# Kernel optimization log

Hardware: AMD Instinct MI355X
Metric: run time of the kernel (lower is better)

## Reference

```python
import jax, jax.numpy as jnp
import numpy as np
import math

E = 64    # d_model = 2*feats
FF = 16   # dim_feedforward
F = 32    # feats
W = 100   # window_size
B = 128   # batch
NH = 32   # nhead = feats


def _mha(q_in, kv_in, w_qkv, b_qkv, w_o, b_o):
    # PyTorch nn.MultiheadAttention, seq-first layout [L, B, E]
    wq, wk, wv = jnp.split(w_qkv, 3, axis=0)
    bq, bk, bv = jnp.split(b_qkv, 3)
    q = q_in @ wq.T + bq
    k = kv_in @ wk.T + bk
    v = kv_in @ wv.T + bv
    L, Bb, _ = q.shape
    S = k.shape[0]
    hd = E // NH  # head_dim = 2
    qh = q.reshape(L, Bb, NH, hd)
    kh = k.reshape(S, Bb, NH, hd)
    vh = v.reshape(S, Bb, NH, hd)
    scores = jnp.einsum('lbhd,sbhd->bhls', qh, kh) / math.sqrt(hd)
    attn = jax.nn.softmax(scores, axis=-1)
    out = jnp.einsum('bhls,sbhd->lbhd', attn, vh).reshape(L, Bb, E)
    return out @ w_o.T + b_o


def _ffn(x, w1, b1, w2, b2):
    h = x @ w1.T + b1
    # nn.LeakyReLU(True) => negative_slope=True==1.0 => identity activation
    return h @ w2.T + b2


def _pos_encode(x):
    # pe[t,d] = sin(t*div[d]) + cos(t*div[d])  (both added, as in source)
    div = jnp.exp(jnp.arange(E, dtype=x.dtype) * (-math.log(10000.0) / E))
    pos = jnp.arange(x.shape[0], dtype=x.dtype)[:, None]
    pe = jnp.sin(pos * div) + jnp.cos(pos * div)  # [W, E]
    return x + pe[:, None, :]


def _encode(src, c, tgt, enc_p):
    (qkv_w, qkv_b, out_w, out_b, l1_w, l1_b, l2_w, l2_b) = enc_p
    s = jnp.concatenate([src, c], axis=2) * math.sqrt(F)
    s = _pos_encode(s)
    s = s + _mha(s, s, qkv_w, qkv_b, out_w, out_b)
    s = s + _ffn(s, l1_w, l1_b, l2_w, l2_b)
    t = jnp.tile(tgt, (1, 1, 2))
    return t, s


def _decode(t, mem, dec_p):
    (sa_qkv_w, sa_qkv_b, sa_out_w, sa_out_b,
     ca_qkv_w, ca_qkv_b, ca_out_w, ca_out_b,
     l1_w, l1_b, l2_w, l2_b) = dec_p
    t = t + _mha(t, t, sa_qkv_w, sa_qkv_b, sa_out_w, sa_out_b)
    t = t + _mha(t, mem, ca_qkv_w, ca_qkv_b, ca_out_w, ca_out_b)
    t = t + _ffn(t, l1_w, l1_b, l2_w, l2_b)
    return t


def _forward(src, tgt,
             enc_qkv_w, enc_qkv_b, enc_out_w, enc_out_b, enc_l1_w, enc_l1_b, enc_l2_w, enc_l2_b,
             d1_sa_qkv_w, d1_sa_qkv_b, d1_sa_out_w, d1_sa_out_b,
             d1_ca_qkv_w, d1_ca_qkv_b, d1_ca_out_w, d1_ca_out_b,
             d1_l1_w, d1_l1_b, d1_l2_w, d1_l2_b,
             d2_sa_qkv_w, d2_sa_qkv_b, d2_sa_out_w, d2_sa_out_b,
             d2_ca_qkv_w, d2_ca_qkv_b, d2_ca_out_w, d2_ca_out_b,
             d2_l1_w, d2_l1_b, d2_l2_w, d2_l2_b,
             fcn_w, fcn_b):
    enc_p = (enc_qkv_w, enc_qkv_b, enc_out_w, enc_out_b, enc_l1_w, enc_l1_b, enc_l2_w, enc_l2_b)
    d1_p = (d1_sa_qkv_w, d1_sa_qkv_b, d1_sa_out_w, d1_sa_out_b,
            d1_ca_qkv_w, d1_ca_qkv_b, d1_ca_out_w, d1_ca_out_b,
            d1_l1_w, d1_l1_b, d1_l2_w, d1_l2_b)
    d2_p = (d2_sa_qkv_w, d2_sa_qkv_b, d2_sa_out_w, d2_sa_out_b,
            d2_ca_qkv_w, d2_ca_qkv_b, d2_ca_out_w, d2_ca_out_b,
            d2_l1_w, d2_l1_b, d2_l2_w, d2_l2_b)
    fcn = lambda x: jax.nn.sigmoid(x @ fcn_w.T + fcn_b)

    c = jnp.zeros_like(src)
    t, mem = _encode(src, c, tgt, enc_p)
    x1 = fcn(_decode(t, mem, d1_p))
    c = (x1 - src) ** 2
    t, mem = _encode(src, c, tgt, enc_p)
    x2 = fcn(_decode(t, mem, d2_p))
    return x1, x2


def setup_inputs() -> dict:
    keys = jax.random.split(jax.random.key(0), 40)
    ki = iter(keys)

    def rn(shape, s=0.05):
        return jax.random.normal(next(ki), shape, dtype=jnp.float32) * s

    inp = {}
    inp['src'] = jax.random.normal(next(ki), (W, B, F), dtype=jnp.float32)
    inp['tgt'] = jax.random.normal(next(ki), (W, B, F), dtype=jnp.float32)
    for pfx in ['enc_', 'd1_sa_', 'd1_ca_', 'd2_sa_', 'd2_ca_']:
        inp[pfx + 'qkv_w'] = rn((3 * E, E))
        inp[pfx + 'qkv_b'] = rn((3 * E,))
        inp[pfx + 'out_w'] = rn((E, E))
        inp[pfx + 'out_b'] = rn((E,))
    for pfx in ['enc_', 'd1_', 'd2_']:
        inp[pfx + 'l1_w'] = rn((FF, E))
        inp[pfx + 'l1_b'] = rn((FF,))
        inp[pfx + 'l2_w'] = rn((E, FF))
        inp[pfx + 'l2_b'] = rn((E,))
    inp['fcn_w'] = rn((F, E))
    inp['fcn_b'] = rn((F,))
    return inp


def reference(src, tgt,
              enc_qkv_w, enc_qkv_b, enc_out_w, enc_out_b, enc_l1_w, enc_l1_b, enc_l2_w, enc_l2_b,
              d1_sa_qkv_w, d1_sa_qkv_b, d1_sa_out_w, d1_sa_out_b,
              d1_ca_qkv_w, d1_ca_qkv_b, d1_ca_out_w, d1_ca_out_b,
              d1_l1_w, d1_l1_b, d1_l2_w, d1_l2_b,
              d2_sa_qkv_w, d2_sa_qkv_b, d2_sa_out_w, d2_sa_out_b,
              d2_ca_qkv_w, d2_ca_qkv_b, d2_ca_out_w, d2_ca_out_b,
              d2_l1_w, d2_l1_b, d2_l2_w, d2_l2_b,
              fcn_w, fcn_b):
    return _forward(src, tgt,
                    enc_qkv_w, enc_qkv_b, enc_out_w, enc_out_b, enc_l1_w, enc_l1_b, enc_l2_w, enc_l2_b,
                    d1_sa_qkv_w, d1_sa_qkv_b, d1_sa_out_w, d1_sa_out_b,
                    d1_ca_qkv_w, d1_ca_qkv_b, d1_ca_out_w, d1_ca_out_b,
                    d1_l1_w, d1_l1_b, d1_l2_w, d1_l2_b,
                    d2_sa_qkv_w, d2_sa_qkv_b, d2_sa_out_w, d2_sa_out_b,
                    d2_ca_qkv_w, d2_ca_qkv_b, d2_ca_out_w, d2_ca_out_b,
                    d2_l1_w, d2_l1_b, d2_l2_w, d2_l2_b,
                    fcn_w, fcn_b)
```

## Files before the change

### kernel.cpp

```cpp
#include <hip/hip_runtime.h>
#include <math.h>


#define TPB 1024
#define RH 50
#define SQ32 5.656854249492381f

#ifndef __has_builtin
#define __has_builtin(x) 0
#endif
#if __has_builtin(__builtin_amdgcn_exp2f)
#define EXP2(x) __builtin_amdgcn_exp2f(x)
#else
#define EXP2(x) exp2f(x)
#endif

typedef float v4f __attribute__((ext_vector_type(4)));

struct KParams { const void* p[36]; };

template<int K, int MC>
__device__ __forceinline__ void ldw(const float* __restrict__ Wt, float* __restrict__ Ws, int tid)
{
    constexpr int WP = MC + 4;
    for (int i = tid; i < MC * K; i += TPB) {
        int m = i / K, k = i - m * K;
        Ws[k * WP + m] = Wt[i];
    }
}

template<int K, int WP>
__device__ __forceinline__ void gemm_row(const float* __restrict__ xrow,
                                         const float* __restrict__ wcol, float acc[4])
{
#pragma unroll 4
    for (int k = 0; k < K; ++k) {
        float xv = xrow[k];
        float4 w = *reinterpret_cast<const float4*>(wcol + k * WP);
        acc[0] = fmaf(xv, w.x, acc[0]);
        acc[1] = fmaf(xv, w.y, acc[1]);
        acc[2] = fmaf(xv, w.z, acc[2]);
        acc[3] = fmaf(xv, w.w, acc[3]);
    }
}

__device__ __forceinline__ void proj_q(const float* __restrict__ Xs, const float* __restrict__ W,
                                       const float* __restrict__ Bi, float* __restrict__ Q,
                                       float* __restrict__ RW, int tid)
{
    __syncthreads();
    ldw<64, 64>(W, RW, tid);
    __syncthreads();
    const int r0 = tid >> 4, cg = tid & 15;
    if (r0 < RH) {
        float a[4] = {0, 0, 0, 0};
        gemm_row<64, 68>(Xs + r0 * 68, RW + 4 * cg, a);
        float4 bb = *reinterpret_cast<const float4*>(Bi + 4 * cg);
        *reinterpret_cast<float4*>(Q + r0 * 68 + 4 * cg) =
            make_float4(a[0] + bb.x, a[1] + bb.y, a[2] + bb.z, a[3] + bb.w);
    }
}

__device__ __forceinline__ void proj_kv(const float* __restrict__ Xs, const float* __restrict__ W,
                                        const float* __restrict__ Bi, int off, int base,
                                        float4* __restrict__ KVs, float* __restrict__ RW, int tid)
{
    __syncthreads();
    ldw<64, 64>(W, RW, tid);
    __syncthreads();
    const int r0 = tid >> 4, cg = tid & 15;
    if (r0 < RH) {
        float a[4] = {0, 0, 0, 0};
        gemm_row<64, 68>(Xs + r0 * 68, RW + 4 * cg, a);
        float4 bb = *reinterpret_cast<const float4*>(Bi + 4 * cg);
        int sg = base + r0, h = 2 * cg;
        float* p0 = reinterpret_cast<float*>(KVs + h * 101 + sg);
        float* p1 = reinterpret_cast<float*>(KVs + (h + 1) * 101 + sg);
        *reinterpret_cast<float2*>(p0 + off) = make_float2(a[0] + bb.x, a[1] + bb.y);
        *reinterpret_cast<float2*>(p1 + off) = make_float2(a[2] + bb.z, a[3] + bb.w);
    }
}

__device__ __forceinline__ void kv_publish(float4* __restrict__ g, int* flagme, int stage,
                                           int base, int b, const float4* __restrict__ KVs, int tid)
{
    __syncthreads();
    for (int i = tid; i < 32 * RH; i += TPB) {
        int sl = i >> 5, h = i & 31, sg = base + sl;
        v4f v = *reinterpret_cast<const v4f*>(KVs + h * 101 + sg);
        float4* p = g + ((size_t)b * 100 + sg) * 32 + h;
        asm volatile("global_store_dwordx4 %0, %1, off sc0 sc1" :: "v"(p), "v"(v) : "memory");
    }
    asm volatile("s_waitcnt vmcnt(0)" ::: "memory");
    __syncthreads();
    if (tid == 0)
        asm volatile("global_store_dword %0, %1, off sc0 sc1" :: "v"(flagme), "v"(stage) : "memory");
}

__device__ __forceinline__ void kv_waitread(const float4* __restrict__ g, const int* flagpt,
                                            int stage, int pbase, int b,
                                            float4* __restrict__ KVs, int tid)
{
    if (tid == 0) {
        int f;
        for (;;) {
            asm volatile("global_load_dword %0, %1, off sc0 sc1\n\ts_waitcnt vmcnt(0)"
                         : "=v"(f) : "v"(flagpt) : "memory");
            if (f >= stage) break;
            __builtin_amdgcn_s_sleep(8);
        }
    }
    __syncthreads();
    for (int i = tid; i < 32 * RH; i += TPB) {
        int sl = i >> 5, h = i & 31, sg = pbase + sl;
        const float4* p = g + ((size_t)b * 100 + sg) * 32 + h;
        v4f v;
        asm volatile("global_load_dwordx4 %0, %1, off sc0 sc1\n\ts_waitcnt vmcnt(0)"
                     : "=v"(v) : "v"(p) : "memory");
        *reinterpret_cast<v4f*>(KVs + h * 101 + sg) = v;
    }
    __syncthreads();
}

__device__ __forceinline__ void attn_block(float* __restrict__ Q,
                                           const float4* __restrict__ KVs, int tid)
{
    __syncthreads();
    if (tid < 416) {
        const int h = tid / 13;
        const int g = tid - 13 * h;
        const int lq0 = 4 * g;
        const float4* kv = KVs + h * 101;
        const float SCALE = 0.7071067811865476f * 1.4426950408889634f;
        float q0[4], q1[4];
#pragma unroll
        for (int j = 0; j < 4; ++j) {
            if (lq0 + j < RH) {
                float2 qv = *reinterpret_cast<const float2*>(Q + (lq0 + j) * 68 + 2 * h);
                q0[j] = qv.x * SCALE; q1[j] = qv.y * SCALE;
            } else { q0[j] = 0.f; q1[j] = 0.f; }
        }
        float mx[4] = {-1e30f, -1e30f, -1e30f, -1e30f};
#pragma unroll 4
        for (int s = 0; s < 100; ++s) {
            float4 k = kv[s];
#pragma unroll
            for (int j = 0; j < 4; ++j)
                mx[j] = fmaxf(mx[j], fmaf(q0[j], k.x, q1[j] * k.y));
        }
        float sum[4] = {0, 0, 0, 0}, a0[4] = {0, 0, 0, 0}, a1[4] = {0, 0, 0, 0};
#pragma unroll 4
        for (int s = 0; s < 100; ++s) {
            float4 k = kv[s];
#pragma unroll
            for (int j = 0; j < 4; ++j) {
                float e = EXP2(fmaf(q0[j], k.x, fmaf(q1[j], k.y, -mx[j])));
                sum[j] += e;
                a0[j] = fmaf(e, k.z, a0[j]);
                a1[j] = fmaf(e, k.w, a1[j]);
            }
        }
#pragma unroll
        for (int j = 0; j < 4; ++j) {
            if (lq0 + j < RH) {
                float inv = 1.f / sum[j];
                *reinterpret_cast<float2*>(Q + (lq0 + j) * 68 + 2 * h) =
                    make_float2(a0[j] * inv, a1[j] * inv);
            }
        }
    }
    __syncthreads();
}

__device__ __forceinline__ void proj_out_res(const float* __restrict__ Ain, const float* __restrict__ W,
                                             const float* __restrict__ Bi, float* __restrict__ Sres,
                                             float* __restrict__ RW, int tid)
{
    __syncthreads();
    ldw<64, 64>(W, RW, tid);
    __syncthreads();
    const int r0 = tid >> 4, cg = tid & 15;
    if (r0 < RH) {
        float a[4] = {0, 0, 0, 0};
        gemm_row<64, 68>(Ain + r0 * 68, RW + 4 * cg, a);
        float4 bb = *reinterpret_cast<const float4*>(Bi + 4 * cg);
        float* sp = Sres + r0 * 68 + 4 * cg;
        float4 s0 = *reinterpret_cast<float4*>(sp);
        *reinterpret_cast<float4*>(sp) =
            make_float4(a[0] + bb.x + s0.x, a[1] + bb.y + s0.y,
                        a[2] + bb.z + s0.z, a[3] + bb.w + s0.w);
    }
    __syncthreads();
}

__device__ __forceinline__ void ffn_block(float* __restrict__ X,
                                          const float* __restrict__ W1, const float* __restrict__ B1,
                                          const float* __restrict__ W2, const float* __restrict__ B2,
                                          float* __restrict__ RW, float* __restrict__ H, int tid)
{
    __syncthreads();
    ldw<64, 16>(W1, RW, tid);
    __syncthreads();
    {
        const int r = tid >> 3, lp = tid & 7;
        if (r < RH) {
            float h0 = B1[2 * lp], h1 = B1[2 * lp + 1];
            const float* xrow = X + r * 68;
#pragma unroll 4
            for (int k = 0; k < 64; ++k) {
                float xv = xrow[k];
                h0 = fmaf(xv, RW[k * 20 + 2 * lp], h0);
                h1 = fmaf(xv, RW[k * 20 + 2 * lp + 1], h1);
            }
            H[r * 20 + 2 * lp] = h0;
            H[r * 20 + 2 * lp + 1] = h1;
        }
    }
    __syncthreads();
    ldw<16, 64>(W2, RW, tid);
    __syncthreads();
    const int r0 = tid >> 4, cg = tid & 15;
    if (r0 < RH) {
        float a[4] = {0, 0, 0, 0};
        gemm_row<16, 68>(H + r0 * 20, RW + 4 * cg, a);
        float4 bb = *reinterpret_cast<const float4*>(B2 + 4 * cg);
        float* xp = X + r0 * 68 + 4 * cg;
        float4 u = *reinterpret_cast<float4*>(xp);
        *reinterpret_cast<float4*>(xp) =
            make_float4(a[0] + bb.x + u.x, a[1] + bb.y + u.y,
                        a[2] + bb.z + u.z, a[3] + bb.w + u.w);
    }
    __syncthreads();
}

__global__ __launch_bounds__(TPB) void k_fused(KParams prm, float* __restrict__ outp,
                                               float4* __restrict__ kvx0,
                                               float4* __restrict__ kvx1,
                                               int* __restrict__ flags)
{
    __shared__ float R0[RH * 68];
    __shared__ float R1[RH * 68];
    __shared__ float R3[RH * 68];
    __shared__ float4 KV[32 * 101];
    __shared__ float RW[64 * 68];
    __shared__ float Hs[RH * 20];
    __shared__ float X1s[RH * 36];

    const int tid = threadIdx.x;
    const int b = blockIdx.x & 127;
    const int half = blockIdx.x >> 7;
    const int base = half * RH;
    const int pbase = RH - base;
    int* flagme = flags + (b * 2 + half) * 32;
    int* flagpt = flags + (b * 2 + (1 - half)) * 32;

    const float* src = (const float*)prm.p[0];
    const float* tgt = (const float*)prm.p[1];

    for (int pass = 0; pass < 2; ++pass) {
        const float* Weq  = (const float*)prm.p[2];
        const float* Beq  = (const float*)prm.p[3];
        const float* Weo  = (const float*)prm.p[4];
        const float* Beo  = (const float*)prm.p[5];
        const float* Wel1 = (const float*)prm.p[22];
        const float* Bel1 = (const float*)prm.p[23];
        const float* Wel2 = (const float*)prm.p[24];
        const float* Bel2 = (const float*)prm.p[25];
        const float* Wsa  = (const float*)prm.p[pass ? 14 : 6];
        const float* Bsa  = (const float*)prm.p[pass ? 15 : 7];
        const float* Wsao = (const float*)prm.p[pass ? 16 : 8];
        const float* Bsao = (const float*)prm.p[pass ? 17 : 9];
        const float* Wca  = (const float*)prm.p[pass ? 18 : 10];
        const float* Bca  = (const float*)prm.p[pass ? 19 : 11];
        const float* Wcao = (const float*)prm.p[pass ? 20 : 12];
        const float* Bcao = (const float*)prm.p[pass ? 21 : 13];
        const float* Wdl1 = (const float*)prm.p[pass ? 30 : 26];
        const float* Bdl1 = (const float*)prm.p[pass ? 31 : 27];
        const float* Wdl2 = (const float*)prm.p[pass ? 32 : 28];
        const float* Bdl2 = (const float*)prm.p[pass ? 33 : 29];
        const float* Wf   = (const float*)prm.p[34];
        const float* Bf   = (const float*)prm.p[35];
        float* outx = outp + (pass ? 409600 : 0);

        __syncthreads();
        for (int i = tid; i < RH * 64; i += TPB) {
            int l = i >> 6, d = i & 63;
            int lg = base + l;
            float sv = src[((size_t)lg * 128 + b) * 32 + (d & 31)];
            float v;
            if (d < 32) v = sv;
            else if (pass == 0) v = 0.f;
            else { float df = X1s[l * 36 + (d - 32)] - sv; v = df * df; }
            float div = __expf((float)d * -0.14391156831212787f);
            float pe = 1.4142135623730951f * __sinf((float)lg * div + 0.7853981633974483f);
            R0[l * 68 + d] = v * SQ32 + pe;
        }

        int st = pass * 3 + 1;
        float4* g = (st & 1) ? kvx1 : kvx0;
        proj_kv(R0, Weq + 4096, Beq + 64, 0, base, KV, RW, tid);
        proj_kv(R0, Weq + 8192, Beq + 128, 2, base, KV, RW, tid);
        kv_publish(g, flagme, st, base, b, KV, tid);
        proj_q(R0, Weq, Beq, R1, RW, tid);
        kv_waitread(g, flagpt, st, pbase, b, KV, tid);
        attn_block(R1, KV, tid);
        proj_out_res(R1, Weo, Beo, R0, RW, tid);
        ffn_block(R0, Wel1, Bel1, Wel2, Bel2, RW, Hs, tid);

        for (int i = tid; i < RH * 8; i += TPB) {
            int l = i >> 3, q4 = i & 7;
            int lg = base + l;
            float4 tv = *reinterpret_cast<const float4*>(tgt + ((size_t)lg * 128 + b) * 32 + 4 * q4);
            *reinterpret_cast<float4*>(R3 + l * 68 + 4 * q4) = tv;
            *reinterpret_cast<float4*>(R3 + l * 68 + 32 + 4 * q4) = tv;
        }

        st = pass * 3 + 2;
        g = (st & 1) ? kvx1 : kvx0;
        proj_kv(R3, Wsa + 4096, Bsa + 64, 0, base, KV, RW, tid);
        proj_kv(R3, Wsa + 8192, Bsa + 128, 2, base, KV, RW, tid);
        kv_publish(g, flagme, st, base, b, KV, tid);
        proj_q(R3, Wsa, Bsa, R1, RW, tid);
        kv_waitread(g, flagpt, st, pbase, b, KV, tid);
        attn_block(R1, KV, tid);
        proj_out_res(R1, Wsao, Bsao, R3, RW, tid);

        st = pass * 3 + 3;
        g = (st & 1) ? kvx1 : kvx0;
        proj_kv(R0, Wca + 4096, Bca + 64, 0, base, KV, RW, tid);
        proj_kv(R0, Wca + 8192, Bca + 128, 2, base, KV, RW, tid);
        kv_publish(g, flagme, st, base, b, KV, tid);
        proj_q(R3, Wca, Bca, R1, RW, tid);
        kv_waitread(g, flagpt, st, pbase, b, KV, tid);
        attn_block(R1, KV, tid);
        proj_out_res(R1, Wcao, Bcao, R3, RW, tid);
        ffn_block(R3, Wdl1, Bdl1, Wdl2, Bdl2, RW, Hs, tid);

        ldw<64, 32>(Wf, RW, tid);
        __syncthreads();
        {
            const int r = tid >> 3, lp = tid & 7;
            if (r < RH) {
                float a[4] = {0, 0, 0, 0};
                gemm_row<64, 36>(R3 + r * 68, RW + 4 * lp, a);
                float4 bb = *reinterpret_cast<const float4*>(Bf + 4 * lp);
                float o0 = 1.f / (1.f + __expf(-(a[0] + bb.x)));
                float o1 = 1.f / (1.f + __expf(-(a[1] + bb.y)));
                float o2 = 1.f / (1.f + __expf(-(a[2] + bb.z)));
                float o3 = 1.f / (1.f + __expf(-(a[3] + bb.w)));
                int rg = base + r;
                *reinterpret_cast<float4*>(outx + ((size_t)rg * 128 + b) * 32 + 4 * lp) =
                    make_float4(o0, o1, o2, o3);
                if (pass == 0)
                    *reinterpret_cast<float4*>(X1s + r * 36 + 4 * lp) =
                        make_float4(o0, o1, o2, o3);
            }
        }
    }
}

extern "C" void kernel_launch(void* const* d_in, const int* in_sizes, int n_in,
                              void* d_out, int out_size, void* d_ws, size_t ws_size,
                              hipStream_t stream)
{
    KParams prm;
    for (int i = 0; i < 36; ++i) prm.p[i] = d_in[i];
    float4* kvx0 = (float4*)d_ws;
    float4* kvx1 = kvx0 + 409600;
    int* flags = (int*)(kvx1 + 409600);
    k_fused<<<dim3(256), dim3(TPB), 0, stream>>>(prm, (float*)d_out, kvx0, kvx1, flags);
}
```

Measured before the change: 184.2 us.

## Pre-transpose weights in a prep kernel and read them from global memory in the fused kernel

A new prep kernel transposes all weight matrices once into workspace, so the fused kernel no longer copies each weight into shared memory behind barriers. The GEMMs now give each thread two rows with packed FMA and read weights straight from global memory (cache). K and V are published in separate buffers directly from the projection, which removes the separate publish pass. The attention tiling also changes to 7 queries per thread across 256 threads. The cost is an extra kernel launch and global or cache-latency-bound weight reads in place of shared-memory reads.

```diff
diff --git a/kernel.cpp b/kernel.cpp
--- a/kernel.cpp
+++ b/kernel.cpp
@@ -15,234 +15,270 @@
 #define EXP2(x) exp2f(x)
 #endif
 
+typedef float v2f __attribute__((ext_vector_type(2)));
 typedef float v4f __attribute__((ext_vector_type(4)));
 
 struct KParams { const void* p[36]; };
 
-template<int K, int MC>
-__device__ __forceinline__ void ldw(const float* __restrict__ Wt, float* __restrict__ Ws, int tid)
-{
-    constexpr int WP = MC + 4;
-    for (int i = tid; i < MC * K; i += TPB) {
-        int m = i / K, k = i - m * K;
-        Ws[k * WP + m] = Wt[i];
+#define WT_QKV(i) (12288 * (i))
+#define WT_OUT(i) (61440 + 4096 * (i))
+#define WT_L1(i)  (81920 + 1024 * (i))
+#define WT_L2(i)  (84992 + 1024 * (i))
+#define WT_FCN    88064
+
+static __device__ const int g_tbl[17][4] = {
+    {2, 192, 6, 0},     {6, 192, 6, 12288}, {10, 192, 6, 24576},
+    {14, 192, 6, 36864},{18, 192, 6, 49152},
+    {4, 64, 6, 61440},  {8, 64, 6, 65536},  {12, 64, 6, 69632},
+    {16, 64, 6, 73728}, {20, 64, 6, 77824},
+    {22, 16, 6, 81920}, {26, 16, 6, 82944}, {30, 16, 6, 83968},
+    {24, 64, 4, 84992}, {28, 64, 4, 86016}, {32, 64, 4, 87040},
+    {34, 32, 6, 88064}};
+
+__global__ __launch_bounds__(256) void k_prep(KParams prm, float* __restrict__ wt)
+{
+    const int e = blockIdx.x;
+    const float* src = (const float*)prm.p[g_tbl[e][0]];
+    const int M = g_tbl[e][1], ks = g_tbl[e][2], dst = g_tbl[e][3];
+    const int N = M << ks, km = (1 << ks) - 1;
+    for (int i = threadIdx.x; i < N; i += 256) {
+        int m = i >> ks, k = i & km;
+        wt[dst + k * M + m] = src[i];
     }
 }
 
 template<int K, int WP>
-__device__ __forceinline__ void gemm_row(const float* __restrict__ xrow,
-                                         const float* __restrict__ wcol, float acc[4])
+__device__ __forceinline__ void gemm24(const float* __restrict__ x0,
+                                       const float* __restrict__ x1,
+                                       const float* __restrict__ gw, v2f acc[4])
 {
 #pragma unroll 4
-    for (int k = 0; k < K; ++k) {
-        float xv = xrow[k];
-        float4 w = *reinterpret_cast<const float4*>(wcol + k * WP);
-        acc[0] = fmaf(xv, w.x, acc[0]);
-        acc[1] = fmaf(xv, w.y, acc[1]);
-        acc[2] = fmaf(xv, w.z, acc[2]);
-        acc[3] = fmaf(xv, w.w, acc[3]);
-    }
-}
-
-__device__ __forceinline__ void proj_q(const float* __restrict__ Xs, const float* __restrict__ W,
-                                       const float* __restrict__ Bi, float* __restrict__ Q,
-                                       float* __restrict__ RW, int tid)
-{
-    __syncthreads();
-    ldw<64, 64>(W, RW, tid);
-    __syncthreads();
+    for (int kk = 0; kk < K / 4; ++kk) {
+        v4f xa = *reinterpret_cast<const v4f*>(x0 + 4 * kk);
+        v4f xb = *reinterpret_cast<const v4f*>(x1 + 4 * kk);
+#pragma unroll
+        for (int j = 0; j < 4; ++j) {
+            v4f w = *reinterpret_cast<const v4f*>(gw + (size_t)(4 * kk + j) * WP);
+            v2f xj = {xa[j], xb[j]};
+#pragma unroll
+            for (int c = 0; c < 4; ++c) {
+                v2f wc = {w[c], w[c]};
+                acc[c] = __builtin_elementwise_fma(xj, wc, acc[c]);
+            }
+        }
+    }
+}
+
+template<int K, int WP>
+__device__ __forceinline__ void gemm14(const float* __restrict__ x,
+                                       const float* __restrict__ gw, float acc[4])
+{
+#pragma unroll 4
+    for (int kk = 0; kk < K / 4; ++kk) {
+        v4f xv = *reinterpret_cast<const v4f*>(x + 4 * kk);
+#pragma unroll
+        for (int j = 0; j < 4; ++j) {
+            v4f w = *reinterpret_cast<const v4f*>(gw + (size_t)(4 * kk + j) * WP);
+#pragma unroll
+            for (int c = 0; c < 4; ++c) acc[c] = fmaf(xv[j], w[c], acc[c]);
+        }
+    }
+}
+
+__device__ __forceinline__ void kv_stage(const float* __restrict__ Xkv,
+    const float* __restrict__ gw ,
+    const float* __restrict__ Bi, int b, int base,
+    float2* __restrict__ Ks, float2* __restrict__ Vs,
+    float2* __restrict__ Kg, float2* __restrict__ Vg, int tid)
+{
+    if (tid >= 800) return;
+    const int c = (tid >= 400) ? 2 : 1;
+    const int u = tid - ((c == 2) ? 400 : 0);
+    const int r0 = u >> 4, cg = u & 15;
+    v2f acc[4] = {};
+    gemm24<64, 192>(Xkv + r0 * 68, Xkv + (r0 + 25) * 68, gw + c * 64 + 4 * cg, acc);
+    v4f bb = *reinterpret_cast<const v4f*>(Bi + c * 64 + 4 * cg);
+    float2* Ls = (c == 1) ? Ks : Vs;
+    float2* Lg = (c == 1) ? Kg : Vg;
+    const int h0 = 2 * cg;
+#pragma unroll
+    for (int rr = 0; rr < 2; ++rr) {
+        int sg = base + r0 + 25 * rr;
+        float2 p0 = make_float2(acc[0][rr] + bb[0], acc[1][rr] + bb[1]);
+        float2 p1 = make_float2(acc[2][rr] + bb[2], acc[3][rr] + bb[3]);
+        Ls[h0 * 102 + sg] = p0;
+        Ls[(h0 + 1) * 102 + sg] = p1;
+        v4f gv = {p0.x, p0.y, p1.x, p1.y};
+        float2* gp = Lg + ((size_t)b * 100 + sg) * 32 + h0;
+        asm volatile("global_store_dwordx4 %0, %1, off sc0 sc1" :: "v"(gp), "v"(gv) : "memory");
+    }
+}
+
+__device__ __forceinline__ void flag_pub(int* flagme, int st, int tid)
+{
+    asm volatile("s_waitcnt vmcnt(0)" ::: "memory");
+    __syncthreads();
+    if (tid == 0)
+        asm volatile("global_store_dword %0, %1, off sc0 sc1" :: "v"(flagme), "v"(st) : "memory");
+}
+
+__device__ __forceinline__ void q_stage(const float* __restrict__ Xq,
+    const float* __restrict__ gw, const float* __restrict__ Bi,
+    float* __restrict__ Q, int tid)
+{
+    if (tid >= 400) return;
     const int r0 = tid >> 4, cg = tid & 15;
-    if (r0 < RH) {
-        float a[4] = {0, 0, 0, 0};
-        gemm_row<64, 68>(Xs + r0 * 68, RW + 4 * cg, a);
-        float4 bb = *reinterpret_cast<const float4*>(Bi + 4 * cg);
-        *reinterpret_cast<float4*>(Q + r0 * 68 + 4 * cg) =
-            make_float4(a[0] + bb.x, a[1] + bb.y, a[2] + bb.z, a[3] + bb.w);
-    }
-}
-
-__device__ __forceinline__ void proj_kv(const float* __restrict__ Xs, const float* __restrict__ W,
-                                        const float* __restrict__ Bi, int off, int base,
-                                        float4* __restrict__ KVs, float* __restrict__ RW, int tid)
-{
-    __syncthreads();
-    ldw<64, 64>(W, RW, tid);
-    __syncthreads();
-    const int r0 = tid >> 4, cg = tid & 15;
-    if (r0 < RH) {
-        float a[4] = {0, 0, 0, 0};
-        gemm_row<64, 68>(Xs + r0 * 68, RW + 4 * cg, a);
-        float4 bb = *reinterpret_cast<const float4*>(Bi + 4 * cg);
-        int sg = base + r0, h = 2 * cg;
-        float* p0 = reinterpret_cast<float*>(KVs + h * 101 + sg);
-        float* p1 = reinterpret_cast<float*>(KVs + (h + 1) * 101 + sg);
-        *reinterpret_cast<float2*>(p0 + off) = make_float2(a[0] + bb.x, a[1] + bb.y);
-        *reinterpret_cast<float2*>(p1 + off) = make_float2(a[2] + bb.z, a[3] + bb.w);
-    }
-}
-
-__device__ __forceinline__ void kv_publish(float4* __restrict__ g, int* flagme, int stage,
-                                           int base, int b, const float4* __restrict__ KVs, int tid)
-{
-    __syncthreads();
-    for (int i = tid; i < 32 * RH; i += TPB) {
-        int sl = i >> 5, h = i & 31, sg = base + sl;
-        v4f v = *reinterpret_cast<const v4f*>(KVs + h * 101 + sg);
-        float4* p = g + ((size_t)b * 100 + sg) * 32 + h;
-        asm volatile("global_store_dwordx4 %0, %1, off sc0 sc1" :: "v"(p), "v"(v) : "memory");
-    }
-    asm volatile("s_waitcnt vmcnt(0)" ::: "memory");
-    __syncthreads();
-    if (tid == 0)
-        asm volatile("global_store_dword %0, %1, off sc0 sc1" :: "v"(flagme), "v"(stage) : "memory");
-}
-
-__device__ __forceinline__ void kv_waitread(const float4* __restrict__ g, const int* flagpt,
-                                            int stage, int pbase, int b,
-                                            float4* __restrict__ KVs, int tid)
+    v2f acc[4] = {};
+    gemm24<64, 192>(Xq + r0 * 68, Xq + (r0 + 25) * 68, gw + 4 * cg, acc);
+    v4f bb = *reinterpret_cast<const v4f*>(Bi + 4 * cg);
+#pragma unroll
+    for (int rr = 0; rr < 2; ++rr) {
+        v4f o = {acc[0][rr] + bb[0], acc[1][rr] + bb[1],
+                 acc[2][rr] + bb[2], acc[3][rr] + bb[3]};
+        *reinterpret_cast<v4f*>(Q + (r0 + 25 * rr) * 68 + 4 * cg) = o;
+    }
+}
+
+__device__ __forceinline__ void kv_wait(const int* flagpt, int st,
+    const float2* __restrict__ Kg, const float2* __restrict__ Vg,
+    int b, int pbase, float2* __restrict__ Ks, float2* __restrict__ Vs, int tid)
 {
     if (tid == 0) {
         int f;
         for (;;) {
             asm volatile("global_load_dword %0, %1, off sc0 sc1\n\ts_waitcnt vmcnt(0)"
                          : "=v"(f) : "v"(flagpt) : "memory");
-            if (f >= stage) break;
+            if (f >= st) break;
             __builtin_amdgcn_s_sleep(8);
         }
     }
     __syncthreads();
-    for (int i = tid; i < 32 * RH; i += TPB) {
-        int sl = i >> 5, h = i & 31, sg = pbase + sl;
-        const float4* p = g + ((size_t)b * 100 + sg) * 32 + h;
+    for (int i = tid; i < 1600; i += TPB) {
+        const int isV = i >= 800;
+        const int j = i - (isV ? 800 : 0);
+        const int sl = j >> 4, hp = j & 15;
+        const int sg = pbase + sl;
+        const float2* gp = (isV ? Vg : Kg) + ((size_t)b * 100 + sg) * 32 + 2 * hp;
         v4f v;
         asm volatile("global_load_dwordx4 %0, %1, off sc0 sc1\n\ts_waitcnt vmcnt(0)"
-                     : "=v"(v) : "v"(p) : "memory");
-        *reinterpret_cast<v4f*>(KVs + h * 101 + sg) = v;
+                     : "=v"(v) : "v"(gp) : "memory");
+        float2* Ls = isV ? Vs : Ks;
+        Ls[(2 * hp) * 102 + sg] = make_float2(v[0], v[1]);
+        Ls[(2 * hp + 1) * 102 + sg] = make_float2(v[2], v[3]);
     }
     __syncthreads();
 }
 
 __device__ __forceinline__ void attn_block(float* __restrict__ Q,
-                                           const float4* __restrict__ KVs, int tid)
-{
-    __syncthreads();
-    if (tid < 416) {
-        const int h = tid / 13;
-        const int g = tid - 13 * h;
-        const int lq0 = 4 * g;
-        const float4* kv = KVs + h * 101;
+    const float2* __restrict__ Ks, const float2* __restrict__ Vs, int tid)
+{
+    if (tid < 256) {
+        const int h = tid >> 3, g = tid & 7;
+        const int lq0 = 7 * g;
+        const int nq = (lq0 + 7 <= RH) ? 7 : (RH - lq0);
+        const v4f* K4 = reinterpret_cast<const v4f*>(Ks + h * 102);
+        const v4f* V4 = reinterpret_cast<const v4f*>(Vs + h * 102);
         const float SCALE = 0.7071067811865476f * 1.4426950408889634f;
-        float q0[4], q1[4];
-#pragma unroll
-        for (int j = 0; j < 4; ++j) {
-            if (lq0 + j < RH) {
-                float2 qv = *reinterpret_cast<const float2*>(Q + (lq0 + j) * 68 + 2 * h);
-                q0[j] = qv.x * SCALE; q1[j] = qv.y * SCALE;
-            } else { q0[j] = 0.f; q1[j] = 0.f; }
-        }
-        float mx[4] = {-1e30f, -1e30f, -1e30f, -1e30f};
-#pragma unroll 4
-        for (int s = 0; s < 100; ++s) {
-            float4 k = kv[s];
-#pragma unroll
-            for (int j = 0; j < 4; ++j)
-                mx[j] = fmaxf(mx[j], fmaf(q0[j], k.x, q1[j] * k.y));
-        }
-        float sum[4] = {0, 0, 0, 0}, a0[4] = {0, 0, 0, 0}, a1[4] = {0, 0, 0, 0};
-#pragma unroll 4
-        for (int s = 0; s < 100; ++s) {
-            float4 k = kv[s];
-#pragma unroll
-            for (int j = 0; j < 4; ++j) {
-                float e = EXP2(fmaf(q0[j], k.x, fmaf(q1[j], k.y, -mx[j])));
-                sum[j] += e;
-                a0[j] = fmaf(e, k.z, a0[j]);
-                a1[j] = fmaf(e, k.w, a1[j]);
+        float q0[7], q1[7], mx[7], sum[7], a0[7], a1[7];
+#pragma unroll
+        for (int j = 0; j < 7; ++j) {
+            float2 qv = (j < nq) ? *reinterpret_cast<const float2*>(Q + (lq0 + j) * 68 + 2 * h)
+                                 : make_float2(0.f, 0.f);
+            q0[j] = qv.x * SCALE; q1[j] = qv.y * SCALE;
+            mx[j] = -1e30f; sum[j] = 0.f; a0[j] = 0.f; a1[j] = 0.f;
+        }
+        for (int s2 = 0; s2 < 50; ++s2) {
+            v4f kp = K4[s2];
+#pragma unroll
+            for (int j = 0; j < 7; ++j) {
+                mx[j] = fmaxf(mx[j], fmaf(q0[j], kp[0], q1[j] * kp[1]));
+                mx[j] = fmaxf(mx[j], fmaf(q0[j], kp[2], q1[j] * kp[3]));
             }
         }
-#pragma unroll
-        for (int j = 0; j < 4; ++j) {
-            if (lq0 + j < RH) {
+        for (int s2 = 0; s2 < 50; ++s2) {
+            v4f kp = K4[s2];
+            v4f vp = V4[s2];
+#pragma unroll
+            for (int j = 0; j < 7; ++j) {
+                float e0 = EXP2(fmaf(q0[j], kp[0], fmaf(q1[j], kp[1], -mx[j])));
+                float e1 = EXP2(fmaf(q0[j], kp[2], fmaf(q1[j], kp[3], -mx[j])));
+                sum[j] += e0 + e1;
+                a0[j] = fmaf(e0, vp[0], fmaf(e1, vp[2], a0[j]));
+                a1[j] = fmaf(e0, vp[1], fmaf(e1, vp[3], a1[j]));
+            }
+        }
+#pragma unroll
+        for (int j = 0; j < 7; ++j)
+            if (j < nq) {
                 float inv = 1.f / sum[j];
                 *reinterpret_cast<float2*>(Q + (lq0 + j) * 68 + 2 * h) =
                     make_float2(a0[j] * inv, a1[j] * inv);
             }
-        }
-    }
-    __syncthreads();
-}
-
-__device__ __forceinline__ void proj_out_res(const float* __restrict__ Ain, const float* __restrict__ W,
-                                             const float* __restrict__ Bi, float* __restrict__ Sres,
-                                             float* __restrict__ RW, int tid)
-{
-    __syncthreads();
-    ldw<64, 64>(W, RW, tid);
-    __syncthreads();
+    }
+}
+
+__device__ __forceinline__ void out_res(const float* __restrict__ Ain,
+    const float* __restrict__ gw, const float* __restrict__ Bi,
+    float* __restrict__ Sres, int tid)
+{
+    if (tid >= 400) return;
     const int r0 = tid >> 4, cg = tid & 15;
-    if (r0 < RH) {
+    v2f acc[4] = {};
+    gemm24<64, 64>(Ain + r0 * 68, Ain + (r0 + 25) * 68, gw + 4 * cg, acc);
+    v4f bb = *reinterpret_cast<const v4f*>(Bi + 4 * cg);
+#pragma unroll
+    for (int rr = 0; rr < 2; ++rr) {
+        float* sp = Sres + (r0 + 25 * rr) * 68 + 4 * cg;
+        v4f s0 = *reinterpret_cast<v4f*>(sp);
+        *reinterpret_cast<v4f*>(sp) =
+            (v4f){acc[0][rr] + bb[0] + s0[0], acc[1][rr] + bb[1] + s0[1],
+                  acc[2][rr] + bb[2] + s0[2], acc[3][rr] + bb[3] + s0[3]};
+    }
+}
+
+__device__ __forceinline__ void ffn_block(float* __restrict__ X,
+    const float* __restrict__ w1, const float* __restrict__ B1,
+    const float* __restrict__ w2, const float* __restrict__ B2,
+    float* __restrict__ Hs, int tid)
+{
+    __syncthreads();
+    if (tid < 200) {
+        const int r = tid >> 2, c4 = tid & 3;
         float a[4] = {0, 0, 0, 0};
-        gemm_row<64, 68>(Ain + r0 * 68, RW + 4 * cg, a);
-        float4 bb = *reinterpret_cast<const float4*>(Bi + 4 * cg);
-        float* sp = Sres + r0 * 68 + 4 * cg;
-        float4 s0 = *reinterpret_cast<float4*>(sp);
-        *reinterpret_cast<float4*>(sp) =
-            make_float4(a[0] + bb.x + s0.x, a[1] + bb.y + s0.y,
-                        a[2] + bb.z + s0.z, a[3] + bb.w + s0.w);
-    }
-    __syncthreads();
-}
-
-__device__ __forceinline__ void ffn_block(float* __restrict__ X,
-                                          const float* __restrict__ W1, const float* __restrict__ B1,
-                                          const float* __restrict__ W2, const float* __restrict__ B2,
-                                          float* __restrict__ RW, float* __restrict__ H, int tid)
-{
-    __syncthreads();
-    ldw<64, 16>(W1, RW, tid);
-    __syncthreads();
-    {
-        const int r = tid >> 3, lp = tid & 7;
-        if (r < RH) {
-            float h0 = B1[2 * lp], h1 = B1[2 * lp + 1];
-            const float* xrow = X + r * 68;
-#pragma unroll 4
-            for (int k = 0; k < 64; ++k) {
-                float xv = xrow[k];
-                h0 = fmaf(xv, RW[k * 20 + 2 * lp], h0);
-                h1 = fmaf(xv, RW[k * 20 + 2 * lp + 1], h1);
-            }
-            H[r * 20 + 2 * lp] = h0;
-            H[r * 20 + 2 * lp + 1] = h1;
-        }
-    }
-    __syncthreads();
-    ldw<16, 64>(W2, RW, tid);
-    __syncthreads();
-    const int r0 = tid >> 4, cg = tid & 15;
-    if (r0 < RH) {
-        float a[4] = {0, 0, 0, 0};
-        gemm_row<16, 68>(H + r0 * 20, RW + 4 * cg, a);
-        float4 bb = *reinterpret_cast<const float4*>(B2 + 4 * cg);
-        float* xp = X + r0 * 68 + 4 * cg;
-        float4 u = *reinterpret_cast<float4*>(xp);
-        *reinterpret_cast<float4*>(xp) =
-            make_float4(a[0] + bb.x + u.x, a[1] + bb.y + u.y,
-                        a[2] + bb.z + u.z, a[3] + bb.w + u.w);
+        gemm14<64, 16>(X + r * 68, w1 + 4 * c4, a);
+        v4f bb = *reinterpret_cast<const v4f*>(B1 + 4 * c4);
+        *reinterpret_cast<v4f*>(Hs + r * 20 + 4 * c4) =
+            (v4f){a[0] + bb[0], a[1] + bb[1], a[2] + bb[2], a[3] + bb[3]};
+    }
+    __syncthreads();
+    if (tid < 400) {
+        const int r0 = tid >> 4, cg = tid & 15;
+        v2f acc[4] = {};
+        gemm24<16, 64>(Hs + r0 * 20, Hs + (r0 + 25) * 20, w2 + 4 * cg, acc);
+        v4f bb = *reinterpret_cast<const v4f*>(B2 + 4 * cg);
+#pragma unroll
+        for (int rr = 0; rr < 2; ++rr) {
+            float* xp = X + (r0 + 25 * rr) * 68 + 4 * cg;
+            v4f u = *reinterpret_cast<v4f*>(xp);
+            *reinterpret_cast<v4f*>(xp) =
+                (v4f){acc[0][rr] + bb[0] + u[0], acc[1][rr] + bb[1] + u[1],
+                      acc[2][rr] + bb[2] + u[2], acc[3][rr] + bb[3] + u[3]};
+        }
     }
     __syncthreads();
 }
 
 __global__ __launch_bounds__(TPB) void k_fused(KParams prm, float* __restrict__ outp,
-                                               float4* __restrict__ kvx0,
-                                               float4* __restrict__ kvx1,
-                                               int* __restrict__ flags)
+    const float* __restrict__ WT,
+    float2* __restrict__ kx0, float2* __restrict__ vx0,
+    float2* __restrict__ kx1, float2* __restrict__ vx1,
+    int* __restrict__ flags)
 {
     __shared__ float R0[RH * 68];
     __shared__ float R1[RH * 68];
     __shared__ float R3[RH * 68];
-    __shared__ float4 KV[32 * 101];
-    __shared__ float RW[64 * 68];
+    __shared__ float2 Ks[32 * 102];
+    __shared__ float2 Vs[32 * 102];
     __shared__ float Hs[RH * 20];
     __shared__ float X1s[RH * 36];
 
@@ -252,33 +288,45 @@
     const int base = half * RH;
     const int pbase = RH - base;
     int* flagme = flags + (b * 2 + half) * 32;
-    int* flagpt = flags + (b * 2 + (1 - half)) * 32;
+    int* flagpt = flags + (b * 2 + 1 - half) * 32;
 
     const float* src = (const float*)prm.p[0];
     const float* tgt = (const float*)prm.p[1];
 
+#define ATT_STAGE(Xq, Xkv, WQKV, BQ, st)                                   \
+    {                                                                      \
+        float2* Kg = ((st) & 1) ? kx1 : kx0;                               \
+        float2* Vg = ((st) & 1) ? vx1 : vx0;                               \
+        kv_stage(Xkv, WQKV, BQ, b, base, Ks, Vs, Kg, Vg, tid);             \
+        flag_pub(flagme, st, tid);                                         \
+        q_stage(Xq, WQKV, BQ, R1, tid);                                    \
+        kv_wait(flagpt, st, Kg, Vg, b, pbase, Ks, Vs, tid);                \
+        attn_block(R1, Ks, Vs, tid);                                       \
+        __syncthreads();                                                   \
+    }
+
     for (int pass = 0; pass < 2; ++pass) {
-        const float* Weq  = (const float*)prm.p[2];
+        const float* Wq_enc = WT + WT_QKV(0);
+        const float* Wq_sa  = WT + WT_QKV(pass ? 3 : 1);
+        const float* Wq_ca  = WT + WT_QKV(pass ? 4 : 2);
+        const float* Wo_enc = WT + WT_OUT(0);
+        const float* Wo_sa  = WT + WT_OUT(pass ? 3 : 1);
+        const float* Wo_ca  = WT + WT_OUT(pass ? 4 : 2);
+        const float* W1_enc = WT + WT_L1(0);
+        const float* W2_enc = WT + WT_L2(0);
+        const float* W1_dec = WT + WT_L1(pass ? 2 : 1);
+        const float* W2_dec = WT + WT_L2(pass ? 2 : 1);
+        const float* Wf     = WT + WT_FCN;
         const float* Beq  = (const float*)prm.p[3];
-        const float* Weo  = (const float*)prm.p[4];
         const float* Beo  = (const float*)prm.p[5];
-        const float* Wel1 = (const float*)prm.p[22];
         const float* Bel1 = (const float*)prm.p[23];
-        const float* Wel2 = (const float*)prm.p[24];
         const float* Bel2 = (const float*)prm.p[25];
-        const float* Wsa  = (const float*)prm.p[pass ? 14 : 6];
         const float* Bsa  = (const float*)prm.p[pass ? 15 : 7];
-        const float* Wsao = (const float*)prm.p[pass ? 16 : 8];
         const float* Bsao = (const float*)prm.p[pass ? 17 : 9];
-        const float* Wca  = (const float*)prm.p[pass ? 18 : 10];
         const float* Bca  = (const float*)prm.p[pass ? 19 : 11];
-        const float* Wcao = (const float*)prm.p[pass ? 20 : 12];
         const float* Bcao = (const float*)prm.p[pass ? 21 : 13];
-        const float* Wdl1 = (const float*)prm.p[pass ? 30 : 26];
         const float* Bdl1 = (const float*)prm.p[pass ? 31 : 27];
-        const float* Wdl2 = (const float*)prm.p[pass ? 32 : 28];
         const float* Bdl2 = (const float*)prm.p[pass ? 33 : 29];
-        const float* Wf   = (const float*)prm.p[34];
         const float* Bf   = (const float*)prm.p[35];
         float* outx = outp + (pass ? 409600 : 0);
 
@@ -295,18 +343,6 @@
             float pe = 1.4142135623730951f * __sinf((float)lg * div + 0.7853981633974483f);
             R0[l * 68 + d] = v * SQ32 + pe;
         }
-
-        int st = pass * 3 + 1;
-        float4* g = (st & 1) ? kvx1 : kvx0;
-        proj_kv(R0, Weq + 4096, Beq + 64, 0, base, KV, RW, tid);
-        proj_kv(R0, Weq + 8192, Beq + 128, 2, base, KV, RW, tid);
-        kv_publish(g, flagme, st, base, b, KV, tid);
-        proj_q(R0, Weq, Beq, R1, RW, tid);
-        kv_waitread(g, flagpt, st, pbase, b, KV, tid);
-        attn_block(R1, KV, tid);
-        proj_out_res(R1, Weo, Beo, R0, RW, tid);
-        ffn_block(R0, Wel1, Bel1, Wel2, Bel2, RW, Hs, tid);
-
         for (int i = tid; i < RH * 8; i += TPB) {
             int l = i >> 3, q4 = i & 7;
             int lg = base + l;
@@ -314,49 +350,35 @@
             *reinterpret_cast<float4*>(R3 + l * 68 + 4 * q4) = tv;
             *reinterpret_cast<float4*>(R3 + l * 68 + 32 + 4 * q4) = tv;
         }
-
-        st = pass * 3 + 2;
-        g = (st & 1) ? kvx1 : kvx0;
-        proj_kv(R3, Wsa + 4096, Bsa + 64, 0, base, KV, RW, tid);
-        proj_kv(R3, Wsa + 8192, Bsa + 128, 2, base, KV, RW, tid);
-        kv_publish(g, flagme, st, base, b, KV, tid);
-        proj_q(R3, Wsa, Bsa, R1, RW, tid);
-        kv_waitread(g, flagpt, st, pbase, b, KV, tid);
-        attn_block(R1, KV, tid);
-        proj_out_res(R1, Wsao, Bsao, R3, RW, tid);
-
-        st = pass * 3 + 3;
-        g = (st & 1) ? kvx1 : kvx0;
-        proj_kv(R0, Wca + 4096, Bca + 64, 0, base, KV, RW, tid);
-        proj_kv(R0, Wca + 8192, Bca + 128, 2, base, KV, RW, tid);
-        kv_publish(g, flagme, st, base, b, KV, tid);
-        proj_q(R3, Wca, Bca, R1, RW, tid);
-        kv_waitread(g, flagpt, st, pbase, b, KV, tid);
-        attn_block(R1, KV, tid);
-        proj_out_res(R1, Wcao, Bcao, R3, RW, tid);
-        ffn_block(R3, Wdl1, Bdl1, Wdl2, Bdl2, RW, Hs, tid);
-
-        ldw<64, 32>(Wf, RW, tid);
         __syncthreads();
-        {
+
+        ATT_STAGE(R0, R0, Wq_enc, Beq, pass * 3 + 1)
+        out_res(R1, Wo_enc, Beo, R0, tid);
+        ffn_block(R0, W1_enc, Bel1, W2_enc, Bel2, Hs, tid);
+
+        ATT_STAGE(R3, R3, Wq_sa, Bsa, pass * 3 + 2)
+        out_res(R1, Wo_sa, Bsao, R3, tid);
+        __syncthreads();
+
+        ATT_STAGE(R3, R0, Wq_ca, Bca, pass * 3 + 3)
+        out_res(R1, Wo_ca, Bcao, R3, tid);
+        ffn_block(R3, W1_dec, Bdl1, W2_dec, Bdl2, Hs, tid);
+
+        if (tid < 400) {
             const int r = tid >> 3, lp = tid & 7;
-            if (r < RH) {
-                float a[4] = {0, 0, 0, 0};
-                gemm_row<64, 36>(R3 + r * 68, RW + 4 * lp, a);
-                float4 bb = *reinterpret_cast<const float4*>(Bf + 4 * lp);
-                float o0 = 1.f / (1.f + __expf(-(a[0] + bb.x)));
-                float o1 = 1.f / (1.f + __expf(-(a[1] + bb.y)));
-                float o2 = 1.f / (1.f + __expf(-(a[2] + bb.z)));
-                float o3 = 1.f / (1.f + __expf(-(a[3] + bb.w)));
-                int rg = base + r;
-                *reinterpret_cast<float4*>(outx + ((size_t)rg * 128 + b) * 32 + 4 * lp) =
-                    make_float4(o0, o1, o2, o3);
-                if (pass == 0)
-                    *reinterpret_cast<float4*>(X1s + r * 36 + 4 * lp) =
-                        make_float4(o0, o1, o2, o3);
-            }
-        }
-    }
+            float a[4] = {0, 0, 0, 0};
+            gemm14<64, 32>(R3 + r * 68, Wf + 4 * lp, a);
+            v4f bb = *reinterpret_cast<const v4f*>(Bf + 4 * lp);
+            v4f o;
+#pragma unroll
+            for (int c = 0; c < 4; ++c) o[c] = 1.f / (1.f + __expf(-(a[c] + bb[c])));
+            int rg = base + r;
+            *reinterpret_cast<v4f*>(outx + ((size_t)rg * 128 + b) * 32 + 4 * lp) = o;
+            if (pass == 0)
+                *reinterpret_cast<v4f*>(X1s + r * 36 + 4 * lp) = o;
+        }
+    }
+#undef ATT_STAGE
 }
 
 extern "C" void kernel_launch(void* const* d_in, const int* in_sizes, int n_in,
@@ -365,8 +387,13 @@
 {
     KParams prm;
     for (int i = 0; i < 36; ++i) prm.p[i] = d_in[i];
-    float4* kvx0 = (float4*)d_ws;
-    float4* kvx1 = kvx0 + 409600;
-    int* flags = (int*)(kvx1 + 409600);
-    k_fused<<<dim3(256), dim3(TPB), 0, stream>>>(prm, (float*)d_out, kvx0, kvx1, flags);
-}
+    float* WT = (float*)d_ws;
+    float2* kx0 = (float2*)(WT + 98304);
+    float2* vx0 = kx0 + 409600;
+    float2* kx1 = vx0 + 409600;
+    float2* vx1 = kx1 + 409600;
+    int* flags = (int*)(vx1 + 409600);
+    k_prep<<<dim3(17), dim3(256), 0, stream>>>(prm, WT);
+    k_fused<<<dim3(256), dim3(TPB), 0, stream>>>(prm, (float*)d_out, WT,
+                                                 kx0, vx0, kx1, vx1, flags);
+}
```

After: 393.0 us. 113% more time.
